# Kernel tuning notes

Measured on AMD Instinct MI355X. Metric: run time of the kernel, lower is better.

Reference implementation:

```python
import jax, jax.numpy as jnp
import numpy as np

N, NC, E, S = 65536, 24576, 524288, 256
VAR_DIM, H1, H2, H3, H4 = 6, 128, 128, 256, 128
THRE, EPS = 0.7, 1e-5


def _bn(x, g, b):
    # BatchNorm1d, training-mode batch statistics (biased var), dropout treated as identity
    mu = x.mean(0)
    v = x.var(0)
    return (x - mu) * jax.lax.rsqrt(v + EPS) * g + b


def _gcn_sparse(h, src, dst, ew, W, b):
    # PyG GCNConv with edge weights: add self-loops (weight 1), symmetric normalization
    n = h.shape[0]
    loop = jnp.arange(n)
    s = jnp.concatenate([src, loop])
    d = jnp.concatenate([dst, loop])
    w = jnp.concatenate([ew, jnp.ones((n,), h.dtype)])
    deg = jax.ops.segment_sum(w, d, num_segments=n)
    dinv = jnp.where(deg > 0, jax.lax.rsqrt(deg), 0.0)
    norm = dinv[s] * w * dinv[d]
    xw = h @ W.T  # [n, out]
    out = jax.ops.segment_sum(norm[:, None] * xw[s], d, num_segments=n)
    return out + b


def _gcn_dense(h, A, W, b):
    # GCNConv on a dense binary adjacency (no edge weights), self-loops + sym norm
    n = h.shape[0]
    A_hat = A + jnp.eye(n, dtype=h.dtype)
    deg = A_hat.sum(0)
    dinv = jnp.where(deg > 0, jax.lax.rsqrt(deg), 0.0)
    return dinv[:, None] * (A_hat.T @ ((h @ W.T) * dinv[:, None])) + b


def setup_inputs() -> dict:
    key = jax.random.key(0)
    ks = jax.random.split(key, 10)

    def w(k, o, i):
        return jax.random.normal(k, (o, i), jnp.float32) / np.float32(np.sqrt(i))

    x = jax.random.normal(ks[0], (N, VAR_DIM), jnp.float32)
    edge_attr = jax.random.uniform(ks[1], (E,), jnp.float32)
    scen_adj = jax.random.uniform(ks[2], (S, S), jnp.float32)
    edge_index = jax.random.randint(ks[3], (2, E), 0, N)
    batch = jnp.arange(N) // (N // S)  # sorted node->graph ids, 256 nodes per graph
    mark = jnp.concatenate([jnp.ones((NC,), jnp.int32), jnp.zeros((N - NC,), jnp.int32)])
    return {
        "x": x, "edge_attr": edge_attr, "scen_adj": scen_adj,
        "mlp_var_w": w(ks[4], H1, VAR_DIM), "mlp_var_b": jnp.zeros((H1,), jnp.float32),
        "mlp_con_w": w(ks[5], H1, 1), "mlp_con_b": jnp.zeros((H1,), jnp.float32),
        "conv1_w": w(ks[6], H2, H1), "conv1_b": jnp.zeros((H2,), jnp.float32),
        "conv2_w": w(ks[7], H3, H2), "conv2_b": jnp.zeros((H3,), jnp.float32),
        "conv3_w": w(ks[8], H4, H3), "conv3_b": jnp.zeros((H4,), jnp.float32),
        "bn1_g": jnp.ones((H1,), jnp.float32), "bn1_b": jnp.zeros((H1,), jnp.float32),
        "bn2_g": jnp.ones((H2,), jnp.float32), "bn2_b": jnp.zeros((H2,), jnp.float32),
        "bn3_g": jnp.ones((H3,), jnp.float32), "bn3_b": jnp.zeros((H3,), jnp.float32),
        "mark": mark, "edge_index": edge_index, "batch": batch, "n_con": NC,
    }


def reference(x, edge_attr, scen_adj, mlp_var_w, mlp_var_b, mlp_con_w, mlp_con_b,
              conv1_w, conv1_b, conv2_w, conv2_b, conv3_w, conv3_b,
              bn1_g, bn1_b, bn2_g, bn2_b, bn3_g, bn3_b,
              mark, edge_index, batch, n_con):
    nc = int(n_con)  # mark layout: first nc nodes are constraints (mark==1), rest vars
    con_feat = jnp.tanh(x[:nc, 0:1] @ mlp_con_w.T + mlp_con_b)
    var_feat = jnp.tanh(x[nc:] @ mlp_var_w.T + mlp_var_b)
    h = jnp.concatenate([con_feat, var_feat], axis=0)  # [N, H1], con-first as in torch cat
    h = _bn(h, bn1_g, bn1_b)  # dropout = identity (eval)
    h = _gcn_sparse(h, edge_index[0], edge_index[1], edge_attr, conv1_w, conv1_b)
    h = jnp.tanh(_bn(h, bn2_g, bn2_b))
    s = scen_adj.shape[0]
    sums = jax.ops.segment_sum(h, batch, num_segments=s)
    cnt = jax.ops.segment_sum(jnp.ones((h.shape[0],), h.dtype), batch, num_segments=s)
    pooled = sums / jnp.maximum(cnt, 1.0)[:, None]  # global_mean_pool -> [S, H2]
    A = (scen_adj >= THRE).astype(h.dtype)  # filter_adj + unweighted edges
    f = jnp.tanh(_bn(_gcn_dense(pooled, A, conv2_w, conv2_b), bn3_g, bn3_b))
    feat = jnp.tanh(_gcn_dense(f, A, conv3_w, conv3_b))
    return feat, feat.mean(0)
```

## Files before the change

kernel.cpp:

```cpp
#include <hip/hip_runtime.h>
#include <hip/hip_bf16.h>
#include <cstddef>

#define N_NODES 65536
#define N_EDGES 524288
#define S_GRAPH 256
#define BN_EPS 1e-5f
#define THRE 0.7f

typedef __hip_bfloat16 bf16;
typedef unsigned int uint32;
typedef unsigned char uchar;
typedef unsigned short ushort16;
typedef __attribute__((ext_vector_type(8))) short short8;
typedef __attribute__((ext_vector_type(4))) float f32x4;

__device__ __forceinline__ float blo(uint32 u) { return __uint_as_float(u << 16); }
__device__ __forceinline__ float bhi(uint32 u) { return __uint_as_float(u & 0xffff0000u); }

__device__ __forceinline__ uint32 packbf(float a, float b)
{
    bf16 ha = __float2bfloat16(a), hb = __float2bfloat16(b);
    unsigned short ua, ub;
    __builtin_memcpy(&ua, &ha, 2); __builtin_memcpy(&ub, &hb, 2);
    return (uint32)ua | ((uint32)ub << 16);
}

__device__ __forceinline__ float ftanh(float x)
{
    float e = __builtin_amdgcn_exp2f(x * 2.8853900817779268f);
    return 1.0f - 2.0f * __builtin_amdgcn_rcpf(e + 1.0f);
}

__global__ __launch_bounds__(256) void k_mlp_hist(
    const float* __restrict__ x, const float* __restrict__ wv,
    const float* __restrict__ bv, const float* __restrict__ wc,
    const float* __restrict__ bc, const int* __restrict__ nconp,
    uint32* __restrict__ h0u, float* __restrict__ stats,
    const int* __restrict__ dst, uint32* __restrict__ blkhist,
    const float* __restrict__ scen, float* __restrict__ fcol,
    const float* __restrict__ w1f, uint32* __restrict__ w1bk)
{
    __shared__ float xs[128 * 6];
    __shared__ float sh[256];
    __shared__ uint32 bh[256];
    int t = threadIdx.x;
    int b = blockIdx.x;
    if (b < 512) {
        bh[t] = 0;
        __syncthreads();
        int e0 = b * 1024 + t * 4;
        int4 d4 = *(const int4*)(dst + e0);
        atomicAdd(&bh[d4.x >> 8], 1u);
        atomicAdd(&bh[d4.y >> 8], 1u);
        atomicAdd(&bh[d4.z >> 8], 1u);
        atomicAdd(&bh[d4.w >> 8], 1u);
        __syncthreads();
        blkhist[b * 256 + t] = bh[t];
        return;
    }
    if (b >= 1024) {
        if (b < 1056) {
            int r0 = (b - 1024) * 8;
            float s = 0.f;
            for (int r = r0; r < r0 + 8; r++)
                s += (scen[r * 256 + t] >= THRE) ? 1.0f : 0.0f;
            atomicAdd(&fcol[t], s);
        } else {
            const float4* w4 = (const float4*)w1f;
            uint2* wo = (uint2*)w1bk;
            #pragma unroll
            for (int it = 0; it < 16; it++) {
                int fi = it * 256 + t;
                float4 w = w4[fi];
                wo[fi] = make_uint2(packbf(w.x, w.y), packbf(w.z, w.w));
            }
        }
        return;
    }
    int n0 = (b - 512) * 128;
    if (t < 192) ((float4*)xs)[t] = ((const float4*)(x + (size_t)n0 * 6))[t];
    __syncthreads();

    int nc = *nconp;
    int lane = t & 63, wave = t >> 6;
    int j0 = 2 * lane;
    const float2* wv2 = (const float2*)wv;
    float2 wa0 = wv2[j0 * 3], wa1 = wv2[j0 * 3 + 1], wa2 = wv2[j0 * 3 + 2];
    float2 wb0 = wv2[j0 * 3 + 3], wb1 = wv2[j0 * 3 + 4], wb2 = wv2[j0 * 3 + 5];
    float wc0 = wc[j0], wc1 = wc[j0 + 1], bc0 = bc[j0], bc1 = bc[j0 + 1];
    float bv0 = bv[j0], bv1 = bv[j0 + 1];

    float s0 = 0.f, ss0 = 0.f, s1 = 0.f, ss1 = 0.f;
    #pragma unroll 4
    for (int m = 0; m < 32; m++) {
        int ln = wave * 32 + m;
        int n = n0 + ln;
        const float* xr = &xs[ln * 6];
        float a0, a1;
        if (n < nc) {
            float xv = xr[0];
            a0 = xv * wc0 + bc0; a1 = xv * wc1 + bc1;
        } else {
            float x0 = xr[0], x1 = xr[1], x2 = xr[2], x3 = xr[3], x4 = xr[4], x5 = xr[5];
            a0 = bv0 + x0 * wa0.x + x1 * wa0.y + x2 * wa1.x + x3 * wa1.y + x4 * wa2.x + x5 * wa2.y;
            a1 = bv1 + x0 * wb0.x + x1 * wb0.y + x2 * wb1.x + x3 * wb1.y + x4 * wb2.x + x5 * wb2.y;
        }
        uint32 pk = packbf(ftanh(a0), ftanh(a1));
        h0u[(size_t)n * 64 + lane] = pk;
        float v0 = blo(pk), v1 = bhi(pk);
        s0 += v0; ss0 += v0 * v0; s1 += v1; ss1 += v1 * v1;
    }
    sh[t] = s0; __syncthreads();
    if (t < 64) atomicAdd(&stats[2 * t], sh[t] + sh[t + 64] + sh[t + 128] + sh[t + 192]);
    __syncthreads(); sh[t] = s1; __syncthreads();
    if (t < 64) atomicAdd(&stats[2 * t + 1], sh[t] + sh[t + 64] + sh[t + 128] + sh[t + 192]);
    __syncthreads(); sh[t] = ss0; __syncthreads();
    if (t < 64) atomicAdd(&stats[128 + 2 * t], sh[t] + sh[t + 64] + sh[t + 128] + sh[t + 192]);
    __syncthreads(); sh[t] = ss1; __syncthreads();
    if (t < 64) atomicAdd(&stats[128 + 2 * t + 1], sh[t] + sh[t + 64] + sh[t + 128] + sh[t + 192]);
}

__global__ __launch_bounds__(256) void k_binscan(
    const uint32* __restrict__ blkhist, uint32* __restrict__ blkoff,
    uint32* __restrict__ binsz, uint32* __restrict__ ubase,
    uint32* __restrict__ pbase, int* __restrict__ ctr)
{
    __shared__ uint32 v[512];
    __shared__ uint32 ps[256];
    __shared__ int flag;
    int g = blockIdx.x, t = threadIdx.x;
    v[t]       = blkhist[t * 256 + g];
    v[t + 256] = blkhist[(t + 256) * 256 + g];
    __syncthreads();
    uint32 a0 = v[2 * t], a1 = v[2 * t + 1];
    ps[t] = a0 + a1; __syncthreads();
    for (int o = 1; o < 256; o <<= 1) {
        uint32 u = (t >= o) ? ps[t - o] : 0;
        __syncthreads();
        ps[t] += u;
        __syncthreads();
    }
    uint32 ex = ps[t] - (a0 + a1);
    ((uint2*)blkoff)[g * 256 + t] = make_uint2(ex, ex + a0);
    if (t == 255) atomicExch((int*)&binsz[g], (int)ps[255]);
    __syncthreads();
    if (t == 0) {
        __threadfence();
        flag = (atomicAdd(ctr, 1) == 255) ? 1 : 0;
    }
    __syncthreads();
    if (flag) {
        __threadfence();
        uint32 s = binsz[t];
        ps[t] = s; __syncthreads();
        for (int o = 1; o < 256; o <<= 1) {
            uint32 u = (t >= o) ? ps[t - o] : 0;
            __syncthreads();
            ps[t] += u;
            __syncthreads();
        }
        ubase[t] = ps[t] - s;
        pbase[t] = ps[t] - s + (uint32)t * 768u;
    }
}

__global__ __launch_bounds__(256) void k_scatter(
    const int* __restrict__ src, const int* __restrict__ dst,
    const float* __restrict__ ew, const uint32* __restrict__ blkoff,
    const uint32* __restrict__ ubase, uint2* __restrict__ ebin)
{
    __shared__ uint32 bh[256];
    __shared__ uint32 bo[256];
    int b = blockIdx.x, t = threadIdx.x;
    bh[t] = 0;
    bo[t] = ubase[t] + blkoff[t * 512 + b];
    __syncthreads();
    int e0 = b * 1024 + t * 4;
    int4 d4 = *(const int4*)(dst + e0);
    int4 s4 = *(const int4*)(src + e0);
    float4 w4 = *(const float4*)(ew + e0);
    int bin; uint32 r;
    bin = d4.x >> 8; r = atomicAdd(&bh[bin], 1u);
    ebin[bo[bin] + r] = make_uint2((uint32)s4.x | ((uint32)(d4.x & 255) << 16), __float_as_uint(w4.x));
    bin = d4.y >> 8; r = atomicAdd(&bh[bin], 1u);
    ebin[bo[bin] + r] = make_uint2((uint32)s4.y | ((uint32)(d4.y & 255) << 16), __float_as_uint(w4.y));
    bin = d4.z >> 8; r = atomicAdd(&bh[bin], 1u);
    ebin[bo[bin] + r] = make_uint2((uint32)s4.z | ((uint32)(d4.z & 255) << 16), __float_as_uint(w4.z));
    bin = d4.w >> 8; r = atomicAdd(&bh[bin], 1u);
    ebin[bo[bin] + r] = make_uint2((uint32)s4.w | ((uint32)(d4.w & 255) << 16), __float_as_uint(w4.w));
}

__global__ __launch_bounds__(256) void k_csr(
    const uint2* __restrict__ ebin, const uint32* __restrict__ binsz,
    const uint32* __restrict__ ubase, const uint32* __restrict__ pbase,
    float* __restrict__ dinv, int* __restrict__ rowp, int* __restrict__ cnts,
    int2* __restrict__ epk)
{
    __shared__ uint2 es[3072];
    __shared__ uint32 hist[256];
    __shared__ int sscan[256];
    __shared__ int rloc[256];
    __shared__ float dlv[256];
    int g = blockIdx.x, t = threadIdx.x;
    int start = (int)ubase[g];
    int sz = min((int)binsz[g], 3072);
    int pb = (int)pbase[g];
    hist[t] = 0;
    __syncthreads();
    for (int i = t; i < sz; i += 256) {
        uint2 e = ebin[start + i];
        int dl = (e.x >> 16) & 255;
        uint32 wfix = __float2uint_rn(__uint_as_float(e.y) * 262144.0f);
        uint32 h = atomicAdd(&hist[dl], (1u << 24) | wfix);
        e.x |= (h >> 24) << 24;
        es[i] = e;
    }
    __syncthreads();
    uint32 hv = hist[t];
    int cnt = (int)(hv >> 24);
    float di = rsqrtf((float)(hv & 0xFFFFFFu) * 3.814697265625e-6f + 1.0f);
    dlv[t] = di;
    dinv[g * 256 + t] = di;
    cnts[g * 256 + t] = cnt;
    int pcnt = (cnt + 3) & ~3;
    sscan[t] = pcnt; __syncthreads();
    for (int o = 1; o < 256; o <<= 1) {
        int u = (t >= o) ? sscan[t - o] : 0;
        __syncthreads();
        sscan[t] += u;
        __syncthreads();
    }
    int rl = sscan[t] - pcnt;
    rloc[t] = rl;
    rowp[g * 256 + t] = pb + rl;
    __syncthreads();
    for (int i = t; i < sz; i += 256) {
        uint2 e = es[i];
        int s  = (int)(e.x & 0xFFFFu);
        int dl = (int)((e.x >> 16) & 255u);
        int r  = (int)(e.x >> 24);
        float w = __uint_as_float(e.y) * dlv[dl];
        epk[pb + rloc[dl] + r] = make_int2(s, __float_as_int(w));
    }
    int base = pb + rl;
    for (int q = cnt; q < pcnt; q++) epk[base + q] = make_int2(g * 256 + t, 0);
}

__global__ __launch_bounds__(256) void k_gemm1f(
    const uint32* __restrict__ h0u, const uint32* __restrict__ w1bk,
    const float* __restrict__ g1, const float* __restrict__ bb1,
    const float* __restrict__ stats, ushort16* __restrict__ xws,
    const float* __restrict__ dinv)
{
    __shared__ short hn_s[64 * 136];
    __shared__ short w_s[128 * 136];
    __shared__ float sc[128], sf[128];
    int t = threadIdx.x;
    int blk = blockIdx.x;
    int row0 = blk * 64;

    if (t < 128) {
        float mu  = stats[t] * (1.0f / N_NODES);
        float var = stats[128 + t] * (1.0f / N_NODES) - mu * mu;
        float rs  = rsqrtf(fmaxf(var, 0.f) + BN_EPS);
        float s   = rs * g1[t];
        sc[t] = s;
        sf[t] = bb1[t] - mu * s;
    }
    __syncthreads();

    const uint4* h4 = (const uint4*)(h0u + (size_t)row0 * 64);
    #pragma unroll
    for (int it = 0; it < 4; it++) {
        int slot = it * 256 + t;
        int r = slot >> 4, k0 = (slot & 15) * 8;
        uint4 u = h4[slot];
        uint32 ua[4] = {u.x, u.y, u.z, u.w};
        uint32 o[4];
        #pragma unroll
        for (int m = 0; m < 4; m++) {
            int k = k0 + 2 * m;
            o[m] = packbf(blo(ua[m]) * sc[k] + sf[k], bhi(ua[m]) * sc[k + 1] + sf[k + 1]);
        }
        *(uint4*)&hn_s[r * 136 + k0] = make_uint4(o[0], o[1], o[2], o[3]);
    }
    const uint4* wv4 = (const uint4*)w1bk;
    #pragma unroll
    for (int it = 0; it < 8; it++) {
        int s2 = it * 256 + t;
        int c = s2 >> 4, k0 = (s2 & 15) * 8;
        *(uint4*)&w_s[c * 136 + k0] = wv4[s2];
    }
    __syncthreads();

    int lane = t & 63, wave = t >> 6;
    int m16 = lane & 15, kh = lane >> 4;
    int mbase = wave * 16;
    f32x4 acc[8] = {};
    #pragma unroll
    for (int ks = 0; ks < 4; ks++) {
        short8 a = *(const short8*)&hn_s[(mbase + m16) * 136 + ks * 32 + kh * 8];
        #pragma unroll
        for (int ct = 0; ct < 8; ct++) {
            short8 bfr = *(const short8*)&w_s[(ct * 16 + m16) * 136 + ks * 32 + kh * 8];
            acc[ct] = __builtin_amdgcn_mfma_f32_16x16x32_bf16(a, bfr, acc[ct], 0, 0, 0);
        }
    }
    float dvr[4];
    #pragma unroll
    for (int r = 0; r < 4; r++) dvr[r] = dinv[row0 + mbase + kh * 4 + r];
    #pragma unroll
    for (int ct = 0; ct < 8; ct++) {
        int col = ct * 16 + m16;
        #pragma unroll
        for (int r = 0; r < 4; r++) {
            int row = mbase + kh * 4 + r;
            bf16 hv = __float2bfloat16(acc[ct][r] * dvr[r]);
            unsigned short us; __builtin_memcpy(&us, &hv, 2);
            xws[(size_t)(row0 + row) * 128 + col] = us;
        }
    }
}

__global__ __launch_bounds__(256) void k_gather(
    const int* __restrict__ rowp, const int* __restrict__ cnts,
    const int2* __restrict__ epk, const uint32* __restrict__ xwu,
    const float* __restrict__ dinv, const float2* __restrict__ b1c2,
    uint32* __restrict__ aggu, float* __restrict__ stats2r)
{
    __shared__ float sh[256];
    int t = threadIdx.x, b = blockIdx.x;
    int lane = t & 63, wave = t >> 6;
    float2 bb = b1c2[lane];
    float s0 = 0.f, ss0 = 0.f, s1 = 0.f, ss1 = 0.f;
    for (int it = 0; it < 8; it++) {
        int n = b * 32 + it * 4 + wave;
        int st = rowp[n];
        int pcnt = (cnts[n] + 3) & ~3;
        float di = dinv[n];
        uint32 u0 = xwu[(size_t)n * 64 + lane];
        float ax = di * blo(u0) + bb.x;
        float ay = di * bhi(u0) + bb.y;
        int en = st + pcnt;
        for (int p = st; p < en; p += 4) {
            int2 q0 = epk[p], q1 = epk[p + 1], q2 = epk[p + 2], q3 = epk[p + 3];
            uint32 v0 = xwu[(size_t)q0.x * 64 + lane];
            uint32 v1 = xwu[(size_t)q1.x * 64 + lane];
            uint32 v2 = xwu[(size_t)q2.x * 64 + lane];
            uint32 v3 = xwu[(size_t)q3.x * 64 + lane];
            float w0 = __int_as_float(q0.y), w1 = __int_as_float(q1.y);
            float w2 = __int_as_float(q2.y), w3 = __int_as_float(q3.y);
            ax += w0 * blo(v0) + w1 * blo(v1) + w2 * blo(v2) + w3 * blo(v3);
            ay += w0 * bhi(v0) + w1 * bhi(v1) + w2 * bhi(v2) + w3 * bhi(v3);
        }
        uint32 pk = packbf(ax, ay);
        aggu[(size_t)n * 64 + lane] = pk;
        float v0 = blo(pk), v1 = bhi(pk);
        s0 += v0; ss0 += v0 * v0; s1 += v1; ss1 += v1 * v1;
    }
    float* st2 = stats2r + (b & 7) * 256;
    sh[t] = s0; __syncthreads();
    if (t < 64) atomicAdd(&st2[2 * t], sh[t] + sh[t + 64] + sh[t + 128] + sh[t + 192]);
    __syncthreads(); sh[t] = s1; __syncthreads();
    if (t < 64) atomicAdd(&st2[2 * t + 1], sh[t] + sh[t + 64] + sh[t + 128] + sh[t + 192]);
    __syncthreads(); sh[t] = ss0; __syncthreads();
    if (t < 64) atomicAdd(&st2[128 + 2 * t], sh[t] + sh[t + 64] + sh[t + 128] + sh[t + 192]);
    __syncthreads(); sh[t] = ss1; __syncthreads();
    if (t < 64) atomicAdd(&st2[128 + 2 * t + 1], sh[t] + sh[t + 64] + sh[t + 128] + sh[t + 192]);
}

__global__ __launch_bounds__(512) void k_poolg2(
    const uint32* __restrict__ aggu, const float* __restrict__ stats2r,
    const float* __restrict__ g2, const float* __restrict__ bb2,
    const float* __restrict__ w2, float* __restrict__ z1)
{
    __shared__ float sc[128], sf[128], sh[512], prow[128];
    int t = threadIdx.x, g = blockIdx.x;
    if (t < 128) {
        float su = 0.f, sq = 0.f;
        #pragma unroll
        for (int r = 0; r < 8; r++) {
            su += stats2r[r * 256 + t];
            sq += stats2r[r * 256 + 128 + t];
        }
        float mu  = su * (1.0f / N_NODES);
        float var = sq * (1.0f / N_NODES) - mu * mu;
        float rs  = rsqrtf(fmaxf(var, 0.f) + BN_EPS);
        float s   = rs * g2[t];
        sc[t] = s;
        sf[t] = bb2[t] - mu * s;
    }
    __syncthreads();
    int c = t & 63, grp = t >> 6;
    float c0s = sc[2 * c], c0f = sf[2 * c], c1s = sc[2 * c + 1], c1f = sf[2 * c + 1];
    const uint32* base = aggu + (size_t)g * 256 * 64;
    float s0 = 0.f, s1 = 0.f;
    for (int r = grp * 32; r < grp * 32 + 32; r++) {
        uint32 u = base[r * 64 + c];
        s0 += ftanh(blo(u) * c0s + c0f);
        s1 += ftanh(bhi(u) * c1s + c1f);
    }
    sh[t] = s0; __syncthreads();
    if (t < 64) {
        float acc = 0.f;
        #pragma unroll
        for (int k = 0; k < 8; k++) acc += sh[t + 64 * k];
        prow[2 * t] = acc * (1.0f / 256.0f);
    }
    __syncthreads(); sh[t] = s1; __syncthreads();
    if (t < 64) {
        float acc = 0.f;
        #pragma unroll
        for (int k = 0; k < 8; k++) acc += sh[t + 64 * k];
        prow[2 * t + 1] = acc * (1.0f / 256.0f);
    }
    __syncthreads();
    if (t < 256) {
        float acc = 0.f;
        const float* wr = w2 + t * 128;
        for (int k = 0; k < 128; k++) acc += prow[k] * wr[k];
        z1[g * 256 + t] = acc;
    }
}

__global__ void k_dgcn1(const float* __restrict__ scen, const float* __restrict__ fcol,
                        const float* __restrict__ z1, const float* __restrict__ b2c,
                        float* __restrict__ y1, float* __restrict__ stats3r)
{
    __shared__ float wk[256];
    int i = blockIdx.x, t = threadIdx.x;
    float a = (scen[t * 256 + i] >= THRE) ? 1.0f : 0.0f;
    if (t == i) a += 1.0f;
    wk[t] = a * rsqrtf(fcol[t] + 1.0f);
    __syncthreads();
    float acc = 0.f;
    for (int k = 0; k < 256; k++) acc += wk[k] * z1[k * 256 + t];
    float v = rsqrtf(fcol[i] + 1.0f) * acc + b2c[t];
    y1[i * 256 + t] = v;
    float* s3 = stats3r + (i & 7) * 512;
    atomicAdd(&s3[t], v);
    atomicAdd(&s3[256 + t], v * v);
}

__global__ void k_gemm3(const float* __restrict__ y1, const float* __restrict__ stats3r,
                        const float* __restrict__ g3, const float* __restrict__ bb3,
                        const float* __restrict__ w3, float* __restrict__ z2)
{
    __shared__ float row[256];
    int i = blockIdx.x, t = threadIdx.x;
    for (int c = t; c < 256; c += 128) {
        float s = 0.f, ss = 0.f;
        #pragma unroll
        for (int r = 0; r < 8; r++) {
            s  += stats3r[r * 512 + c];
            ss += stats3r[r * 512 + 256 + c];
        }
        float mu  = s * (1.0f / 256.0f);
        float var = ss * (1.0f / 256.0f) - mu * mu;
        float rs  = rsqrtf(fmaxf(var, 0.f) + BN_EPS);
        float scj = rs * g3[c];
        float sfj = bb3[c] - mu * scj;
        row[c] = ftanh(y1[i * 256 + c] * scj + sfj);
    }
    __syncthreads();
    float acc = 0.f;
    const float* wr = w3 + t * 256;
    for (int k = 0; k < 256; k++) acc += row[k] * wr[k];
    z2[i * 128 + t] = acc;
}

__global__ void k_dgcn2(const float* __restrict__ scen, const float* __restrict__ fcol,
                        const float* __restrict__ z2, const float* __restrict__ b3c,
                        float* __restrict__ out, float* __restrict__ meanr,
                        int* __restrict__ ctr)
{
    __shared__ float wk[256];
    __shared__ int flag;
    int i = blockIdx.x, t = threadIdx.x;
    for (int k = t; k < 256; k += 128) {
        float a = (scen[k * 256 + i] >= THRE) ? 1.0f : 0.0f;
        if (k == i) a += 1.0f;
        wk[k] = a * rsqrtf(fcol[k] + 1.0f);
    }
    __syncthreads();
    float acc = 0.f;
    for (int k = 0; k < 256; k++) acc += wk[k] * z2[k * 128 + t];
    float v = ftanh(rsqrtf(fcol[i] + 1.0f) * acc + b3c[t]);
    out[i * 128 + t] = v;
    atomicAdd(&meanr[(i & 7) * 128 + t], v);
    __syncthreads();
    if (t == 0) {
        __threadfence();
        flag = (atomicAdd(ctr, 1) == 255) ? 1 : 0;
    }
    __syncthreads();
    if (flag) {
        __threadfence();
        float s = 0.f;
        #pragma unroll
        for (int r = 0; r < 8; r++) s += meanr[r * 128 + t];
        out[S_GRAPH * 128 + t] = s * (1.0f / 256.0f);
    }
}

extern "C" void kernel_launch(void* const* d_in, const int* in_sizes, int n_in,
                              void* d_out, int out_size, void* d_ws, size_t ws_size,
                              hipStream_t stream)
{
    const float* x        = (const float*)d_in[0];
    const float* edge_attr= (const float*)d_in[1];
    const float* scen     = (const float*)d_in[2];
    const float* wv       = (const float*)d_in[3];
    const float* bv       = (const float*)d_in[4];
    const float* wc       = (const float*)d_in[5];
    const float* bc       = (const float*)d_in[6];
    const float* w1       = (const float*)d_in[7];
    const float* b1c      = (const float*)d_in[8];
    const float* w2       = (const float*)d_in[9];
    const float* b2c      = (const float*)d_in[10];
    const float* w3       = (const float*)d_in[11];
    const float* b3c      = (const float*)d_in[12];
    const float* g1       = (const float*)d_in[13];
    const float* bb1      = (const float*)d_in[14];
    const float* g2       = (const float*)d_in[15];
    const float* bb2      = (const float*)d_in[16];
    const float* g3       = (const float*)d_in[17];
    const float* bb3      = (const float*)d_in[18];
    const int*  ei        = (const int*)d_in[20];
    const int*  nconp     = (const int*)d_in[22];
    const int*  src = ei;
    const int*  dst = ei + N_EDGES;

    float* wsf = (float*)d_ws;
    uint32*   h0u  = (uint32*)wsf;
    uint32*   aggu = (uint32*)wsf;
    uint32*   xwu  = (uint32*)(wsf + 4194304);
    float* zb      = wsf + 8388608;
    float* stats1  = zb;
    float* stats2r = zb + 512;
    float* stats3r = zb + 2560;
    float* fcol    = zb + 6656;
    float* meanr   = zb + 6912;
    int*   ctrs    = (int*)(zb + 7936);
    const int ZN   = 7944;
    float* deg     = zb + ZN;
    int*   rowp    = (int*)(deg + 65536);
    int*   cnts    = rowp + 65536;
    uint32* blkhist= (uint32*)(cnts + 65536);
    uint32* blkoff = blkhist + 131072;
    uint32* binsz  = blkoff + 131072;
    uint32* ubase  = binsz + 256;
    uint32* pbase  = ubase + 256;
    uint2* ebin    = (uint2*)(pbase + 256);
    int2*  epk     = (int2*)(ebin + 524288);
    uint32* w1bk   = (uint32*)(epk + 720896);
    float* z1      = (float*)(w1bk + 8192);
    float* y1      = z1 + 65536;
    float* z2      = y1 + 65536;

    float* out = (float*)d_out;

    hipMemsetAsync(zb, 0, ZN * sizeof(float), stream);

    k_mlp_hist<<<1057, 256, 0, stream>>>(x, wv, bv, wc, bc, nconp, h0u, stats1,
                                         dst, blkhist, scen, fcol, w1, w1bk);
    k_binscan<<<256, 256, 0, stream>>>(blkhist, blkoff, binsz, ubase, pbase, &ctrs[0]);
    k_scatter<<<512, 256, 0, stream>>>(src, dst, edge_attr, blkoff, ubase, ebin);
    k_csr<<<256, 256, 0, stream>>>(ebin, binsz, ubase, pbase, deg, rowp, cnts, epk);
    k_gemm1f<<<1024, 256, 0, stream>>>(h0u, w1bk, g1, bb1, stats1, (ushort16*)xwu, deg);
    k_gather<<<2048, 256, 0, stream>>>(rowp, cnts, epk, xwu, deg,
                                       (const float2*)b1c, aggu, stats2r);
    k_poolg2<<<S_GRAPH, 512, 0, stream>>>(aggu, stats2r, g2, bb2, w2, z1);
    k_dgcn1<<<256, 256, 0, stream>>>(scen, fcol, z1, b2c, y1, stats3r);
    k_gemm3<<<256, 128, 0, stream>>>(y1, stats3r, g3, bb3, w3, z2);
    k_dgcn2<<<256, 128, 0, stream>>>(scen, fcol, z2, b3c, out, meanr, &ctrs[1]);
}
```

Measured before the change: 253.3 us.

## Drop memset launch, replace stat atomics with partials, unroll gather by eight

Removes the hipMemsetAsync by zeroing the accumulators and counters inside a spare block of the first kernel, and computes the column counts of the scenario adjacency in a single block with plain stores instead of atomics. The BN1 statistics are now written as per-block partial sums and reduced by an extra block added to the binscan kernel, replacing global atomics. The gather inner loop is unrolled to eight neighbours to keep more loads in flight. In exchange the column-count block runs serially over 256 rows, and the stats reduction block reads 512 partial rows.

```diff
diff --git a/kernel.cpp b/kernel.cpp
--- a/kernel.cpp
+++ b/kernel.cpp
@@ -36,10 +36,11 @@
     const float* __restrict__ x, const float* __restrict__ wv,
     const float* __restrict__ bv, const float* __restrict__ wc,
     const float* __restrict__ bc, const int* __restrict__ nconp,
-    uint32* __restrict__ h0u, float* __restrict__ stats,
+    uint32* __restrict__ h0u, float* __restrict__ pstat,
     const int* __restrict__ dst, uint32* __restrict__ blkhist,
     const float* __restrict__ scen, float* __restrict__ fcol,
-    const float* __restrict__ w1f, uint32* __restrict__ w1bk)
+    const float* __restrict__ w1f, uint32* __restrict__ w1bk,
+    float* __restrict__ zacc, int* __restrict__ ctrs)
 {
     __shared__ float xs[128 * 6];
     __shared__ float sh[256];
@@ -60,13 +61,12 @@
         return;
     }
     if (b >= 1024) {
-        if (b < 1056) {
-            int r0 = (b - 1024) * 8;
+        if (b == 1024) {
             float s = 0.f;
-            for (int r = r0; r < r0 + 8; r++)
+            for (int r = 0; r < 256; r++)
                 s += (scen[r * 256 + t] >= THRE) ? 1.0f : 0.0f;
-            atomicAdd(&fcol[t], s);
-        } else {
+            fcol[t] = s;
+        } else if (b == 1056) {
             const float4* w4 = (const float4*)w1f;
             uint2* wo = (uint2*)w1bk;
             #pragma unroll
@@ -75,6 +75,8 @@
                 float4 w = w4[fi];
                 wo[fi] = make_uint2(packbf(w.x, w.y), packbf(w.z, w.w));
             }
+            for (int i = t; i < 7168; i += 256) zacc[i] = 0.f;
+            if (t < 8) ctrs[t] = 0;
         }
         return;
     }
@@ -111,25 +113,33 @@
         float v0 = blo(pk), v1 = bhi(pk);
         s0 += v0; ss0 += v0 * v0; s1 += v1; ss1 += v1 * v1;
     }
+    float* pst = pstat + (size_t)(b - 512) * 256;
     sh[t] = s0; __syncthreads();
-    if (t < 64) atomicAdd(&stats[2 * t], sh[t] + sh[t + 64] + sh[t + 128] + sh[t + 192]);
+    if (t < 64) pst[2 * t] = sh[t] + sh[t + 64] + sh[t + 128] + sh[t + 192];
     __syncthreads(); sh[t] = s1; __syncthreads();
-    if (t < 64) atomicAdd(&stats[2 * t + 1], sh[t] + sh[t + 64] + sh[t + 128] + sh[t + 192]);
+    if (t < 64) pst[2 * t + 1] = sh[t] + sh[t + 64] + sh[t + 128] + sh[t + 192];
     __syncthreads(); sh[t] = ss0; __syncthreads();
-    if (t < 64) atomicAdd(&stats[128 + 2 * t], sh[t] + sh[t + 64] + sh[t + 128] + sh[t + 192]);
+    if (t < 64) pst[128 + 2 * t] = sh[t] + sh[t + 64] + sh[t + 128] + sh[t + 192];
     __syncthreads(); sh[t] = ss1; __syncthreads();
-    if (t < 64) atomicAdd(&stats[128 + 2 * t + 1], sh[t] + sh[t + 64] + sh[t + 128] + sh[t + 192]);
+    if (t < 64) pst[128 + 2 * t + 1] = sh[t] + sh[t + 64] + sh[t + 128] + sh[t + 192];
 }
 
 __global__ __launch_bounds__(256) void k_binscan(
     const uint32* __restrict__ blkhist, uint32* __restrict__ blkoff,
     uint32* __restrict__ binsz, uint32* __restrict__ ubase,
-    uint32* __restrict__ pbase, int* __restrict__ ctr)
+    uint32* __restrict__ pbase, const float* __restrict__ pstat,
+    float* __restrict__ stats, int* __restrict__ ctr)
 {
     __shared__ uint32 v[512];
     __shared__ uint32 ps[256];
     __shared__ int flag;
     int g = blockIdx.x, t = threadIdx.x;
+    if (g == 256) {
+        float acc = 0.f;
+        for (int j = 0; j < 512; j++) acc += pstat[j * 256 + t];
+        stats[t] = acc;
+        return;
+    }
     v[t]       = blkhist[t * 256 + g];
     v[t + 256] = blkhist[(t + 256) * 256 + g];
     __syncthreads();
@@ -343,7 +353,28 @@
         float ax = di * blo(u0) + bb.x;
         float ay = di * bhi(u0) + bb.y;
         int en = st + pcnt;
-        for (int p = st; p < en; p += 4) {
+        int p = st;
+        for (; p + 8 <= en; p += 8) {
+            int2 q0 = epk[p],     q1 = epk[p + 1], q2 = epk[p + 2], q3 = epk[p + 3];
+            int2 q4 = epk[p + 4], q5 = epk[p + 5], q6 = epk[p + 6], q7 = epk[p + 7];
+            uint32 v0 = xwu[(size_t)q0.x * 64 + lane];
+            uint32 v1 = xwu[(size_t)q1.x * 64 + lane];
+            uint32 v2 = xwu[(size_t)q2.x * 64 + lane];
+            uint32 v3 = xwu[(size_t)q3.x * 64 + lane];
+            uint32 v4 = xwu[(size_t)q4.x * 64 + lane];
+            uint32 v5 = xwu[(size_t)q5.x * 64 + lane];
+            uint32 v6 = xwu[(size_t)q6.x * 64 + lane];
+            uint32 v7 = xwu[(size_t)q7.x * 64 + lane];
+            float w0 = __int_as_float(q0.y), w1 = __int_as_float(q1.y);
+            float w2 = __int_as_float(q2.y), w3 = __int_as_float(q3.y);
+            float w4 = __int_as_float(q4.y), w5 = __int_as_float(q5.y);
+            float w6 = __int_as_float(q6.y), w7 = __int_as_float(q7.y);
+            ax += w0 * blo(v0) + w1 * blo(v1) + w2 * blo(v2) + w3 * blo(v3);
+            ay += w0 * bhi(v0) + w1 * bhi(v1) + w2 * bhi(v2) + w3 * bhi(v3);
+            ax += w4 * blo(v4) + w5 * blo(v5) + w6 * blo(v6) + w7 * blo(v7);
+            ay += w4 * bhi(v4) + w5 * bhi(v5) + w6 * bhi(v6) + w7 * bhi(v7);
+        }
+        if (p < en) {
             int2 q0 = epk[p], q1 = epk[p + 1], q2 = epk[p + 2], q3 = epk[p + 3];
             uint32 v0 = xwu[(size_t)q0.x * 64 + lane];
             uint32 v1 = xwu[(size_t)q1.x * 64 + lane];
@@ -538,13 +569,13 @@
     uint32*   xwu  = (uint32*)(wsf + 4194304);
     float* zb      = wsf + 8388608;
     float* stats1  = zb;
-    float* stats2r = zb + 512;
-    float* stats3r = zb + 2560;
-    float* fcol    = zb + 6656;
-    float* meanr   = zb + 6912;
+    float* zacc    = zb + 512;
+    float* stats2r = zacc;
+    float* stats3r = zacc + 2048;
+    float* meanr   = zacc + 6144;
+    float* fcol    = zb + 7680;
     int*   ctrs    = (int*)(zb + 7936);
-    const int ZN   = 7944;
-    float* deg     = zb + ZN;
+    float* deg     = zb + 7944;
     int*   rowp    = (int*)(deg + 65536);
     int*   cnts    = rowp + 65536;
     uint32* blkhist= (uint32*)(cnts + 65536);
@@ -558,14 +589,15 @@
     float* z1      = (float*)(w1bk + 8192);
     float* y1      = z1 + 65536;
     float* z2      = y1 + 65536;
+    float* pstat   = z2 + 32768;
 
     float* out = (float*)d_out;
 
-    hipMemsetAsync(zb, 0, ZN * sizeof(float), stream);
-
-    k_mlp_hist<<<1057, 256, 0, stream>>>(x, wv, bv, wc, bc, nconp, h0u, stats1,
-                                         dst, blkhist, scen, fcol, w1, w1bk);
-    k_binscan<<<256, 256, 0, stream>>>(blkhist, blkoff, binsz, ubase, pbase, &ctrs[0]);
+    k_mlp_hist<<<1057, 256, 0, stream>>>(x, wv, bv, wc, bc, nconp, h0u, pstat,
+                                         dst, blkhist, scen, fcol, w1, w1bk,
+                                         zacc, ctrs);
+    k_binscan<<<257, 256, 0, stream>>>(blkhist, blkoff, binsz, ubase, pbase,
+                                       pstat, stats1, &ctrs[0]);
     k_scatter<<<512, 256, 0, stream>>>(src, dst, edge_attr, blkoff, ubase, ebin);
     k_csr<<<256, 256, 0, stream>>>(ebin, binsz, ubase, pbase, deg, rowp, cnts, epk);
     k_gemm1f<<<1024, 256, 0, stream>>>(h0u, w1bk, g1, bb1, stats1, (ushort16*)xwu, deg);
```

New measurement: 238.8 us. 1.06x faster.
